# Performance work log

Measured on AMD Instinct MI355X. Metric: run time of the kernel, lower is better.

Reference implementation:

```python
import jax, jax.numpy as jnp
import numpy as np

FP8_MAX = 448.0  # max normal of float8_e4m3fn
NUM_HEADS = 16


def act_quant(x):
    # per-tensor fp8 quantization: scale so max|x| maps to FP8_MAX
    scale = jnp.max(jnp.abs(x)) / FP8_MAX
    q = (x / scale).astype(jnp.float8_e4m3fn)
    return q, scale


def setup_inputs() -> dict:
    key = jax.random.key(0)
    k1, k2, k3, k4 = jax.random.split(key, 4)
    B, S, H = 2, 2048, 2048
    x = jax.random.normal(k1, (B, S, H), dtype=jnp.float32)
    W_qkv = jax.random.normal(k2, (H, 3 * H), dtype=jnp.float32) * (1.0 / np.sqrt(H))
    W_out = jax.random.normal(k3, (H, H), dtype=jnp.float32) * (1.0 / np.sqrt(H))
    b_out = jnp.zeros((H,), dtype=jnp.float32)
    return {"x": x, "W_qkv": W_qkv, "W_out": W_out, "b_out": b_out}


def reference(x, W_qkv, W_out, b_out):
    B, S, H = x.shape
    nH = NUM_HEADS
    hd = H // nH  # 128, matches head_dim default used for scaling

    qkv = jnp.einsum('bsh,hf->bsf', x, W_qkv)          # [B,S,3H]
    qkv = qkv.reshape(B, S, 3, nH, hd)
    q = qkv[:, :, 0].transpose(0, 2, 1, 3)             # [B,nH,S,hd]
    k = qkv[:, :, 1].transpose(0, 2, 1, 3)
    v = qkv[:, :, 2].transpose(0, 2, 1, 3)

    q8, q_scale = act_quant(q)
    k8, k_scale = act_quant(k)
    # fp8_gemm_optimized: dequantized GEMM = (a @ b) * a_scale * b_scale
    scores = jnp.einsum('bhqd,bhkd->bhqk',
                        q8.astype(jnp.float32), k8.astype(jnp.float32))
    scores = scores * (q_scale * k_scale) / jnp.sqrt(jnp.float32(hd))

    attn = jax.nn.softmax(scores, axis=-1)             # [B,nH,S,S]
    # (dropout omitted: deterministic / eval mode)

    v8, v_scale = act_quant(v)
    out = jnp.einsum('bhqk,bhkd->bhqd', attn, v8.astype(jnp.float32))
    out = out * v_scale                                # a_scale = 1 for attn weights

    out = out.transpose(0, 2, 1, 3).reshape(B, S, H)
    return jnp.einsum('bsh,ho->bso', out, W_out) + b_out
```

## Files before the change

kernel.cpp:

```cpp
#include <hip/hip_runtime.h>
#include <hip/hip_bf16.h>
#include <math.h>

#define B_   2
#define S_   2048
#define H_   2048
#define NH   16
#define HD   128
#define ROWS (B_ * S_)
#define F3   (3 * H_)
#define KS   2048

typedef _Float16 f16x8 __attribute__((ext_vector_type(8)));
typedef float    f32x4  __attribute__((ext_vector_type(4)));
typedef float    f32x16 __attribute__((ext_vector_type(16)));

union H2 { unsigned u; _Float16 h[2]; };
union H4 { ushort4 s4; _Float16 h[4]; };
union H4b { uint2 u2; _Float16 h[4]; };
union PU { unsigned u[4]; f16x8 v8; };

__device__ __forceinline__ void gl_lds16(const void* g, void* l) {
  __builtin_amdgcn_global_load_lds(
      (const __attribute__((address_space(1))) void*)g,
      (__attribute__((address_space(3))) void*)l, 16, 0, 0);
}

__device__ __forceinline__ float quant_e4m3(float x) {
  float ax = fabsf(x);
  float q;
  if (ax < 0.015625f) {
    q = rintf(ax * 512.0f) * (1.0f / 512.0f);
  } else {
    unsigned eb = __float_as_uint(ax) & 0x7f800000u;
    float quantum = __uint_as_float(eb - (3u << 23));
    q = rintf(ax / quantum) * quantum;
    if (q > 448.0f) q = 448.0f;
  }
  return copysignf(q, x);
}

__global__ __launch_bounds__(256) void prep_split(
    const float* __restrict__ x, const float* __restrict__ Wqkv,
    _Float16* __restrict__ A1hi, _Float16* __restrict__ A1lo,
    _Float16* __restrict__ B1thi, _Float16* __restrict__ B1tlo) {
  __shared__ _Float16 ht[64][72];
  __shared__ _Float16 lt[64][72];
  const int t = threadIdx.x;
  const int bid = blockIdx.x;
  if (bid < 8192) {
    const size_t i = (size_t)bid * 256 + t;
    float4 v = ((const float4*)x)[i];
    H4 h, l;
    h.h[0] = (_Float16)v.x; l.h[0] = (_Float16)(v.x - (float)h.h[0]);
    h.h[1] = (_Float16)v.y; l.h[1] = (_Float16)(v.y - (float)h.h[1]);
    h.h[2] = (_Float16)v.z; l.h[2] = (_Float16)(v.z - (float)h.h[2]);
    h.h[3] = (_Float16)v.w; l.h[3] = (_Float16)(v.w - (float)h.h[3]);
    ((ushort4*)A1hi)[i] = h.s4;
    ((ushort4*)A1lo)[i] = l.s4;
  } else {
    const int idx = bid - 8192;
    const int n0 = (idx % 96) * 64, k0 = (idx / 96) * 64;
    const int K = H_, N = F3;
#pragma unroll
    for (int p = 0; p < 4; p++) {
      const int k = p * 16 + (t >> 4);
      const int n = (t & 15) * 4;
      float4 v = *(const float4*)(Wqkv + (size_t)(k0 + k) * N + n0 + n);
      _Float16 h0 = (_Float16)v.x, h1 = (_Float16)v.y,
               h2 = (_Float16)v.z, h3 = (_Float16)v.w;
      ht[n + 0][k] = h0; lt[n + 0][k] = (_Float16)(v.x - (float)h0);
      ht[n + 1][k] = h1; lt[n + 1][k] = (_Float16)(v.y - (float)h1);
      ht[n + 2][k] = h2; lt[n + 2][k] = (_Float16)(v.z - (float)h2);
      ht[n + 3][k] = h3; lt[n + 3][k] = (_Float16)(v.w - (float)h3);
    }
    __syncthreads();
#pragma unroll
    for (int it = 0; it < 2; it++) {
      const int idx2 = it * 256 + t;
      const int r = idx2 >> 3, c = (idx2 & 7) * 8;
      *(uint4*)(B1thi + (size_t)(n0 + r) * K + k0 + c) = *(const uint4*)&ht[r][c];
      *(uint4*)(B1tlo + (size_t)(n0 + r) * K + k0 + c) = *(const uint4*)&lt[r][c];
    }
  }
}

__global__ __launch_bounds__(256) void split_tr(
    const float* __restrict__ in, _Float16* __restrict__ hi,
    _Float16* __restrict__ lo, int K, int N) {
  __shared__ _Float16 ht[64][72];
  __shared__ _Float16 lt[64][72];
  const int t = threadIdx.x;
  const int n0 = blockIdx.x * 64, k0 = blockIdx.y * 64;
#pragma unroll
  for (int p = 0; p < 4; p++) {
    const int k = p * 16 + (t >> 4);
    const int n = (t & 15) * 4;
    float4 v = *(const float4*)(in + (size_t)(k0 + k) * N + n0 + n);
    _Float16 h0 = (_Float16)v.x, h1 = (_Float16)v.y,
             h2 = (_Float16)v.z, h3 = (_Float16)v.w;
    ht[n + 0][k] = h0; lt[n + 0][k] = (_Float16)(v.x - (float)h0);
    ht[n + 1][k] = h1; lt[n + 1][k] = (_Float16)(v.y - (float)h1);
    ht[n + 2][k] = h2; lt[n + 2][k] = (_Float16)(v.z - (float)h2);
    ht[n + 3][k] = h3; lt[n + 3][k] = (_Float16)(v.w - (float)h3);
  }
  __syncthreads();
#pragma unroll
  for (int it = 0; it < 2; it++) {
    const int idx = it * 256 + t;
    const int r = idx >> 3, c = (idx & 7) * 8;
    *(uint4*)(hi + (size_t)(n0 + r) * K + k0 + c) = *(const uint4*)&ht[r][c];
    *(uint4*)(lo + (size_t)(n0 + r) * K + k0 + c) = *(const uint4*)&lt[r][c];
  }
}

#define STAGE_A(tt, dst) do {                                                  \
    const _Float16* As_ = ((tt) < 64) ? Ahi : Alo;                             \
    const size_t so_ = (size_t)(row0 + wave * 8 + srow) * KS +                 \
                       (((tt) & 31) << 6) + schunk;                            \
    _Float16* db_ = (dst) + wave * 512;                                        \
    gl_lds16(As_ + so_,                    db_);                               \
    gl_lds16(As_ + so_ + (size_t)64 * KS,  db_ + 4096);                        \
    gl_lds16(As_ + so_ + (size_t)128 * KS, db_ + 8192);                       \
    gl_lds16(As_ + so_ + (size_t)192 * KS, db_ + 12288);                       \
  } while (0)

#define STAGE_B(tt, dst) do {                                                  \
    const _Float16* Bs_ = ((((tt) >> 5)) == 1) ? Btlo : Bthi;                  \
    const size_t so_ = (size_t)(col0 + wave * 8 + srow) * KS +                 \
                       (((tt) & 31) << 6) + schunk;                            \
    _Float16* db_ = (dst) + 16384 + wave * 512;                                \
    gl_lds16(Bs_ + so_,                    db_);                               \
    gl_lds16(Bs_ + so_ + (size_t)64 * KS,  db_ + 4096);                        \
  } while (0)

__global__ __launch_bounds__(512, 2) void gemm_split256(
    const _Float16* __restrict__ Ahi, const _Float16* __restrict__ Alo,
    const _Float16* __restrict__ Bthi, const _Float16* __restrict__ Btlo,
    float* __restrict__ C, const float* __restrict__ bias,
    unsigned* mx, int N, int has_bias) {
  __shared__ __align__(16) _Float16 lds[73728];
  const int t = threadIdx.x;
  const int wave = t >> 6, lane = t & 63;
  const int l15 = lane & 15, g = lane >> 4;
  const int wm = wave >> 1, wn = wave & 1;

  const int gx = gridDim.x;
  const int nwg = gx * gridDim.y;
  const int bid = blockIdx.y * gx + blockIdx.x;
  const int tile = (bid & 7) * (nwg >> 3) + (bid >> 3);
  const int row0 = (tile / gx) * 256, col0 = (tile % gx) * 128;

  const int srow = lane >> 3;
  const int schunk = ((lane & 7) ^ srow) << 3;

  f32x4 acc[4][4] = {};

  _Float16* bufA = lds;
  _Float16* bufB = lds + 24576;
  _Float16* bufC = lds + 49152;

  STAGE_A(0, bufA);
  STAGE_B(0, bufA);
  STAGE_A(1, bufB);
  STAGE_B(1, bufB);
  asm volatile("s_waitcnt vmcnt(6)" ::: "memory");
  __builtin_amdgcn_s_barrier();

  for (int kc = 0; kc < 96; kc++) {
    const _Float16* Ab = bufA;
    const _Float16* Bb = bufA + 16384;
    f16x8 af0[4], bf0[4];
#pragma unroll
    for (int i = 0; i < 4; i++) {
      const int r_ = wm * 64 + i * 16 + l15;
      af0[i] = *(const f16x8*)(Ab + r_ * 64 + ((g ^ (r_ & 7)) << 3));
    }
#pragma unroll
    for (int j = 0; j < 4; j++) {
      const int r_ = wn * 64 + j * 16 + l15;
      bf0[j] = *(const f16x8*)(Bb + r_ * 64 + ((g ^ (r_ & 7)) << 3));
    }
    if (kc + 2 < 96) STAGE_A(kc + 2, bufC);
    __builtin_amdgcn_s_barrier();
    asm volatile("s_waitcnt lgkmcnt(0)" ::: "memory");
    __builtin_amdgcn_sched_barrier(0);
    __builtin_amdgcn_s_setprio(1);
#pragma unroll
    for (int i = 0; i < 4; i++)
#pragma unroll
      for (int j = 0; j < 4; j++)
        acc[i][j] = __builtin_amdgcn_mfma_f32_16x16x32_f16(af0[i], bf0[j], acc[i][j], 0, 0, 0);
    __builtin_amdgcn_s_setprio(0);
    __builtin_amdgcn_s_barrier();
    f16x8 af1[4], bf1[4];
#pragma unroll
    for (int i = 0; i < 4; i++) {
      const int r_ = wm * 64 + i * 16 + l15;
      af1[i] = *(const f16x8*)(Ab + r_ * 64 + (((4 ^ g) ^ (r_ & 7)) << 3));
    }
#pragma unroll
    for (int j = 0; j < 4; j++) {
      const int r_ = wn * 64 + j * 16 + l15;
      bf1[j] = *(const f16x8*)(Bb + r_ * 64 + (((4 ^ g) ^ (r_ & 7)) << 3));
    }
    if (kc + 2 < 96) STAGE_B(kc + 2, bufC);
    __builtin_amdgcn_s_barrier();
    asm volatile("s_waitcnt lgkmcnt(0)" ::: "memory");
    __builtin_amdgcn_sched_barrier(0);
    __builtin_amdgcn_s_setprio(1);
#pragma unroll
    for (int i = 0; i < 4; i++)
#pragma unroll
      for (int j = 0; j < 4; j++)
        acc[i][j] = __builtin_amdgcn_mfma_f32_16x16x32_f16(af1[i], bf1[j], acc[i][j], 0, 0, 0);
    __builtin_amdgcn_s_setprio(0);
    if (kc < 94) { asm volatile("s_waitcnt vmcnt(6)" ::: "memory"); }
    else         { asm volatile("s_waitcnt vmcnt(0)" ::: "memory"); }
    __builtin_amdgcn_s_barrier();
    _Float16* tmp = bufA; bufA = bufB; bufB = bufC; bufC = tmp;
  }

  float bmax = 0.0f;
#pragma unroll
  for (int j = 0; j < 4; j++) {
    const int col = col0 + wn * 64 + j * 16 + l15;
    const float bv = has_bias ? bias[col] : 0.0f;
#pragma unroll
    for (int i = 0; i < 4; i++) {
      const int rbase = row0 + wm * 64 + i * 16 + g * 4;
#pragma unroll
      for (int r = 0; r < 4; r++) {
        const float v = acc[i][j][r] + bv;
        C[(size_t)(rbase + r) * N + col] = v;
        bmax = fmaxf(bmax, fabsf(v));
      }
    }
  }

  if (mx) {
    __syncthreads();
    float* red = (float*)lds;
    red[t] = bmax;
    __syncthreads();
    for (int s2 = 256; s2 > 0; s2 >>= 1) {
      if (t < s2) red[t] = fmaxf(red[t], red[t + s2]);
      __syncthreads();
    }
    if (t == 0) atomicMax(mx + (col0 >> 11), __float_as_uint(red[0]));
  }
}

__global__ __launch_bounds__(256) void quant_qkv(
    const float* __restrict__ qkv, const unsigned* __restrict__ mx,
    _Float16* __restrict__ q8, _Float16* __restrict__ k8,
    _Float16* __restrict__ v8t) {
  __shared__ _Float16 tile[64 * 72];
  const int t = threadIdx.x;
  const int bid = blockIdx.x;

  if (bid < 16384) {
    const size_t base = ((size_t)bid * 256 + t) * 4;
    const int row = (int)(base >> 12);
    const int col = (int)(base & 4095);
    const int seg = col >> 11;
    const int c2 = col & 2047;
    const int h = c2 >> 7, d = c2 & 127;
    const int b = row >> 11, s = row & 2047;
    const float scale = __uint_as_float(mx[seg]) / 448.0f;
    float4 v = *(const float4*)(qkv + (size_t)row * F3 + col);
    H4 r;
    r.h[0] = (_Float16)quant_e4m3(v.x / scale);
    r.h[1] = (_Float16)quant_e4m3(v.y / scale);
    r.h[2] = (_Float16)quant_e4m3(v.z / scale);
    r.h[3] = (_Float16)quant_e4m3(v.w / scale);
    _Float16* dst = seg ? k8 : q8;
    const size_t di = ((size_t)((b * NH + h) * S_) + s) * HD + d;
    *(ushort4*)(dst + di) = r.s4;
  } else {
    const int bt = bid - 16384;
    const int dtile = bt & 1;
    const int stile = (bt >> 1) & 31;
    const int bh = bt >> 6;
    const int b = bh >> 4, h = bh & 15;
    const int s0 = stile * 64, d0 = dtile * 64;
    const float scale = __uint_as_float(mx[2]) / 448.0f;

#pragma unroll
    for (int r = 0; r < 4; r++) {
      const int s = s0 + r * 16 + (t >> 4);
      const int dl = (t & 15) * 4;
      float4 v = *(const float4*)(qkv + (size_t)(b * S_ + s) * F3 + 4096 + h * HD + d0 + dl);
      tile[(dl + 0) * 72 + r * 16 + (t >> 4)] = (_Float16)quant_e4m3(v.x / scale);
      tile[(dl + 1) * 72 + r * 16 + (t >> 4)] = (_Float16)quant_e4m3(v.y / scale);
      tile[(dl + 2) * 72 + r * 16 + (t >> 4)] = (_Float16)quant_e4m3(v.z / scale);
      tile[(dl + 3) * 72 + r * 16 + (t >> 4)] = (_Float16)quant_e4m3(v.w / scale);
    }
    __syncthreads();
#pragma unroll
    for (int j = 0; j < 2; j++) {
      const int wi = j * 256 + t;
      const int dl = wi >> 3;
      const int sch = (wi & 7) * 8;
      uint4 val = *(const uint4*)(tile + dl * 72 + sch);
      *(uint4*)(v8t + (size_t)bh * (HD * S_) + (size_t)(d0 + dl) * S_ + s0 + sch) = val;
    }
  }
}

__global__ __launch_bounds__(256, 2) void attn_kernel(
    const _Float16* __restrict__ q8, const _Float16* __restrict__ k8,
    const _Float16* __restrict__ v8t, const unsigned* __restrict__ mx,
    _Float16* __restrict__ oHi, _Float16* __restrict__ oLo) {
  __shared__ __align__(16) char ldsb[65536];

  const int t = threadIdx.x;
  const int wave = t >> 6;
  const int lane = t & 63;
  const int l31 = lane & 31;
  const int hf = lane >> 5;

  const int qt = blockIdx.x & 15;
  const int bh = blockIdx.x >> 4;
  const int b = bh >> 4, h = bh & 15;
  const int q0 = qt * 128 + wave * 32;

  const float qs = __uint_as_float(mx[0]) * (1.0f / 448.0f);
  const float ks = __uint_as_float(mx[1]) * (1.0f / 448.0f);
  const float vs = __uint_as_float(mx[2]) * (1.0f / 448.0f);
  const float sfac = qs * ks * 0.08838834764831843f;

  f16x8 qf[8];
  {
    const _Float16* qp = q8 + ((size_t)(bh * S_) + q0 + l31) * HD + hf * 8;
#pragma unroll
    for (int st = 0; st < 8; st++)
      qf[st] = *(const f16x8*)(qp + st * 16);
  }

  f32x16 acc[4] = {};
  float m_base = 0.0f;
  float l_run = 0.0f;

  const size_t kB_ = (size_t)(bh * S_) * HD;
  const size_t vB_ = (size_t)bh * (HD * S_);
  const int k_key = t >> 4;
  const int k_dch = (t & 15) * 8;
  const int k_wch = (((t & 15) ^ (k_key & 7)) << 3);
  const int v_d   = t >> 3;
  const int v_sch = (t & 7) * 8;
  const int v_wch = (((t & 7) ^ (v_d & 7)) << 3);

  const int NT = S_ / 64;
  uint4 kp[4], vp[4];

#pragma unroll
  for (int r = 0; r < 4; r++)
    kp[r] = *(const uint4*)(k8 + kB_ + (size_t)(r * 16 + k_key) * HD + k_dch);
#pragma unroll
  for (int r = 0; r < 4; r++)
    vp[r] = *(const uint4*)(v8t + vB_ + (size_t)(r * 32 + v_d) * S_ + v_sch);
  {
    _Float16* K0 = (_Float16*)ldsb;
    _Float16* V0 = (_Float16*)(ldsb + 32768);
#pragma unroll
    for (int r = 0; r < 4; r++)
      *(uint4*)(K0 + (r * 16 + k_key) * 128 + k_wch) = kp[r];
#pragma unroll
    for (int r = 0; r < 4; r++)
      *(uint4*)(V0 + (r * 32 + v_d) * 64 + v_wch) = vp[r];
  }
#pragma unroll
  for (int r = 0; r < 4; r++)
    kp[r] = *(const uint4*)(k8 + kB_ + (size_t)(64 + r * 16 + k_key) * HD + k_dch);
#pragma unroll
  for (int r = 0; r < 4; r++)
    vp[r] = *(const uint4*)(v8t + vB_ + (size_t)(r * 32 + v_d) * S_ + 64 + v_sch);
  __syncthreads();

  for (int kt = 0; kt < NT; kt++) {
    const _Float16* Klds  = (const _Float16*)(ldsb + (kt & 1) * 16384);
    const _Float16* VTlds = (const _Float16*)(ldsb + 32768 + (kt & 1) * 16384);
    if (kt + 1 < NT) {
      _Float16* Kn = (_Float16*)(ldsb + ((kt + 1) & 1) * 16384);
      _Float16* Vn = (_Float16*)(ldsb + 32768 + ((kt + 1) & 1) * 16384);
#pragma unroll
      for (int r = 0; r < 4; r++)
        *(uint4*)(Kn + (r * 16 + k_key) * 128 + k_wch) = kp[r];
#pragma unroll
      for (int r = 0; r < 4; r++)
        *(uint4*)(Vn + (r * 32 + v_d) * 64 + v_wch) = vp[r];
    }
    if (kt + 2 < NT) {
      const int nk = (kt + 2) * 64;
#pragma unroll
      for (int r = 0; r < 4; r++)
        kp[r] = *(const uint4*)(k8 + kB_ + (size_t)(nk + r * 16 + k_key) * HD + k_dch);
#pragma unroll
      for (int r = 0; r < 4; r++)
        vp[r] = *(const uint4*)(v8t + vB_ + (size_t)(r * 32 + v_d) * S_ + nk + v_sch);
    }

#pragma unroll
    for (int sub = 0; sub < 2; sub++) {
      const int ksub = sub * 32;
      f32x16 s = {};
      __builtin_amdgcn_s_setprio(1);
#pragma unroll
      for (int st = 0; st < 8; st++) {
        const int krow = ksub + l31;
        f16x8 af = *(const f16x8*)(Klds + krow * 128 +
                                   (((st * 2 + hf) ^ (krow & 7)) << 3));
        s = __builtin_amdgcn_mfma_f32_32x32x16_f16(af, qf[st], s, 0, 0, 0);
      }
      __builtin_amdgcn_s_setprio(0);
      f16x8 vf0 = *(const f16x8*)(VTlds + l31 * 64 +
                                  (((sub * 4 + 0 * 2 + hf) ^ (l31 & 7)) << 3));
      f16x8 vf1 = *(const f16x8*)(VTlds + l31 * 64 +
                                  (((sub * 4 + 1 * 2 + hf) ^ (l31 & 7)) << 3));
      float p[16];
      if (kt == 0 && sub == 0) {
        float tmax = -3.0e38f;
#pragma unroll
        for (int i = 0; i < 16; i++) {
          p[i] = s[i] * sfac;
          tmax = fmaxf(tmax, p[i]);
        }
        tmax = fmaxf(tmax, __shfl_xor(tmax, 32));
        m_base = tmax;
        float rs = 0.0f;
#pragma unroll
        for (int i = 0; i < 16; i++) {
          p[i] = __expf(p[i] - tmax);
          rs += p[i];
        }
        l_run += rs;
      } else {
        const float mb = m_base;
        float rs = 0.0f;
#pragma unroll
        for (int i = 0; i < 16; i++) {
          p[i] = fminf(__expf(fmaf(s[i], sfac, -mb)), 60000.0f);
          rs += p[i];
        }
        l_run += rs;
      }
      f16x8 pf[2];
#pragma unroll
      for (int c = 0; c < 2; c++) {
        const int c8 = c * 8;
        const int sidx = hf ? 0 : 4;
        const int oidx = hf ? 4 : 0;
        H2 s0h, s1h, o0h, o1h;
        s0h.h[0] = (_Float16)p[c8 + sidx];     s0h.h[1] = (_Float16)p[c8 + sidx + 1];
        s1h.h[0] = (_Float16)p[c8 + sidx + 2]; s1h.h[1] = (_Float16)p[c8 + sidx + 3];
        o0h.h[0] = (_Float16)p[c8 + oidx];     o0h.h[1] = (_Float16)p[c8 + oidx + 1];
        o1h.h[0] = (_Float16)p[c8 + oidx + 2]; o1h.h[1] = (_Float16)p[c8 + oidx + 3];
        unsigned r0 = (unsigned)__shfl_xor((int)s0h.u, 32);
        unsigned r1 = (unsigned)__shfl_xor((int)s1h.u, 32);
        PU pu;
        if (hf == 0) { pu.u[0] = o0h.u; pu.u[1] = o1h.u; pu.u[2] = r0; pu.u[3] = r1; }
        else         { pu.u[0] = r0;    pu.u[1] = r1;    pu.u[2] = o0h.u; pu.u[3] = o1h.u; }
        pf[c] = pu.v8;
      }
#pragma unroll
      for (int dt = 0; dt < 4; dt++) {
        f16x8 nf0, nf1;
        if (dt < 3) {
          const int vrow = (dt + 1) * 32 + l31;
          nf0 = *(const f16x8*)(VTlds + vrow * 64 +
                                (((sub * 4 + 0 * 2 + hf) ^ (vrow & 7)) << 3));
          nf1 = *(const f16x8*)(VTlds + vrow * 64 +
                                (((sub * 4 + 1 * 2 + hf) ^ (vrow & 7)) << 3));
        }
        __builtin_amdgcn_s_setprio(1);
        acc[dt] = __builtin_amdgcn_mfma_f32_32x32x16_f16(vf0, pf[0], acc[dt], 0, 0, 0);
        acc[dt] = __builtin_amdgcn_mfma_f32_32x32x16_f16(vf1, pf[1], acc[dt], 0, 0, 0);
        __builtin_amdgcn_s_setprio(0);
        vf0 = nf0; vf1 = nf1;
      }
    }
    __syncthreads();
  }

  l_run += __shfl_xor(l_run, 32);
  const float f = vs / l_run;

  _Float16* obuf = (_Float16*)ldsb;
  const int obase = wave * 4352;
#pragma unroll
  for (int pass = 0; pass < 2; pass++) {
    __syncthreads();
#pragma unroll
    for (int dt = 0; dt < 4; dt++) {
#pragma unroll
      for (int iq = 0; iq < 4; iq++) {
        const int dl0 = 8 * iq + 4 * hf;
        H4b w;
#pragma unroll
        for (int e = 0; e < 4; e++) {
          const float o = acc[dt][iq * 4 + e] * f;
          const _Float16 hh = (_Float16)o;
          w.h[e] = pass ? (_Float16)(o - (float)hh) : hh;
        }
        *(uint2*)&obuf[obase + l31 * 136 + dt * 32 + dl0] = w.u2;
      }
    }
    __syncthreads();
    _Float16* dst = pass ? oLo : oHi;
#pragma unroll
    for (int ii = 0; ii < 8; ii++) {
      const int qrow = ii * 4 + (lane >> 4);
      const int ch = (lane & 15) * 8;
      uint4 val = *(const uint4*)&obuf[obase + qrow * 136 + ch];
      const size_t ofs = (size_t)(b * S_ + q0 + qrow) * H_ + h * HD + ch;
      *(uint4*)(dst + ofs) = val;
    }
  }
}

extern "C" void kernel_launch(void* const* d_in, const int* in_sizes, int n_in,
                              void* d_out, int out_size, void* d_ws, size_t ws_size,
                              hipStream_t stream) {
  const float* x     = (const float*)d_in[0];
  const float* W_qkv = (const float*)d_in[1];
  const float* W_out = (const float*)d_in[2];
  const float* b_out = (const float*)d_in[3];
  float* out = (float*)d_out;

  char* ws = (char*)d_ws;
  float*    qkv    = (float*)ws;
  _Float16* A2hi   = (_Float16*)(ws + 33554432);
  _Float16* A2lo   = (_Float16*)(ws + 50331648);
  _Float16* B2thi  = (_Float16*)(ws + 67108864);
  _Float16* B2tlo  = (_Float16*)(ws + 75497472);
  _Float16* B1thi  = (_Float16*)(ws + 100663296);
  _Float16* B1tlo  = (_Float16*)(ws + 125829120);
  _Float16* q8     = (_Float16*)(ws + 100663296);
  _Float16* k8     = (_Float16*)(ws + 117440512);
  _Float16* v8t    = (_Float16*)(ws + 134217728);
  _Float16* A1hi   = (_Float16*)(ws + 150994944);
  _Float16* A1lo   = (_Float16*)(ws + 167772160);
  unsigned* mx     = (unsigned*)(ws + 184549376);

  hipMemsetAsync(mx, 0, 3 * sizeof(unsigned), stream);

  prep_split<<<11264, 256, 0, stream>>>(x, W_qkv, A1hi, A1lo, B1thi, B1tlo);

  gemm_split256<<<dim3(F3 / 128, ROWS / 256), 512, 0, stream>>>(
      A1hi, A1lo, B1thi, B1tlo, qkv, nullptr, mx, F3, 0);

  quant_qkv<<<16384 + B_ * NH * 32 * 2, 256, 0, stream>>>(qkv, mx, q8, k8, v8t);

  attn_kernel<<<B_ * NH * 16, 256, 0, stream>>>(q8, k8, v8t, mx, A2hi, A2lo);

  split_tr<<<dim3(H_ / 64, H_ / 64), 256, 0, stream>>>(W_out, B2thi, B2tlo, H_, H_);

  gemm_split256<<<dim3(H_ / 128, ROWS / 256), 512, 0, stream>>>(
      A2hi, A2lo, B2thi, B2tlo, out, b_out, nullptr, H_, 1);
}
```

Measured before the change: 784.4 us.

## Merge GEMM half-steps and batch both attention key sub-tiles per iteration

In the GEMM main loop, all A/B fragments for both k-halves are now loaded up front and both stage copies issued together. This removes two of the three barriers, the lgkmcnt waits, sched_barriers and setprio toggles per iteration. In the attention kernel, the two 32-key sub-tiles are computed together: both QK^T accumulators are interleaved, softmax runs for both, then the PV MFMAs are issued in one loop. This raises instruction-level parallelism but also register pressure, which could lower occupancy or cause spills.

```diff
diff --git a/kernel.cpp b/kernel.cpp
--- a/kernel.cpp
+++ b/kernel.cpp
@@ -170,51 +170,33 @@
   for (int kc = 0; kc < 96; kc++) {
     const _Float16* Ab = bufA;
     const _Float16* Bb = bufA + 16384;
-    f16x8 af0[4], bf0[4];
+    f16x8 af0[4], bf0[4], af1[4], bf1[4];
 #pragma unroll
     for (int i = 0; i < 4; i++) {
       const int r_ = wm * 64 + i * 16 + l15;
       af0[i] = *(const f16x8*)(Ab + r_ * 64 + ((g ^ (r_ & 7)) << 3));
+      af1[i] = *(const f16x8*)(Ab + r_ * 64 + (((4 ^ g) ^ (r_ & 7)) << 3));
     }
 #pragma unroll
     for (int j = 0; j < 4; j++) {
       const int r_ = wn * 64 + j * 16 + l15;
       bf0[j] = *(const f16x8*)(Bb + r_ * 64 + ((g ^ (r_ & 7)) << 3));
-    }
-    if (kc + 2 < 96) STAGE_A(kc + 2, bufC);
-    __builtin_amdgcn_s_barrier();
-    asm volatile("s_waitcnt lgkmcnt(0)" ::: "memory");
-    __builtin_amdgcn_sched_barrier(0);
-    __builtin_amdgcn_s_setprio(1);
+      bf1[j] = *(const f16x8*)(Bb + r_ * 64 + (((4 ^ g) ^ (r_ & 7)) << 3));
+    }
+    if (kc + 2 < 96) {
+      STAGE_A(kc + 2, bufC);
+      STAGE_B(kc + 2, bufC);
+    }
 #pragma unroll
     for (int i = 0; i < 4; i++)
 #pragma unroll
       for (int j = 0; j < 4; j++)
         acc[i][j] = __builtin_amdgcn_mfma_f32_16x16x32_f16(af0[i], bf0[j], acc[i][j], 0, 0, 0);
-    __builtin_amdgcn_s_setprio(0);
-    __builtin_amdgcn_s_barrier();
-    f16x8 af1[4], bf1[4];
-#pragma unroll
-    for (int i = 0; i < 4; i++) {
-      const int r_ = wm * 64 + i * 16 + l15;
-      af1[i] = *(const f16x8*)(Ab + r_ * 64 + (((4 ^ g) ^ (r_ & 7)) << 3));
-    }
-#pragma unroll
-    for (int j = 0; j < 4; j++) {
-      const int r_ = wn * 64 + j * 16 + l15;
-      bf1[j] = *(const f16x8*)(Bb + r_ * 64 + (((4 ^ g) ^ (r_ & 7)) << 3));
-    }
-    if (kc + 2 < 96) STAGE_B(kc + 2, bufC);
-    __builtin_amdgcn_s_barrier();
-    asm volatile("s_waitcnt lgkmcnt(0)" ::: "memory");
-    __builtin_amdgcn_sched_barrier(0);
-    __builtin_amdgcn_s_setprio(1);
 #pragma unroll
     for (int i = 0; i < 4; i++)
 #pragma unroll
       for (int j = 0; j < 4; j++)
         acc[i][j] = __builtin_amdgcn_mfma_f32_16x16x32_f16(af1[i], bf1[j], acc[i][j], 0, 0, 0);
-    __builtin_amdgcn_s_setprio(0);
     if (kc < 94) { asm volatile("s_waitcnt vmcnt(6)" ::: "memory"); }
     else         { asm volatile("s_waitcnt vmcnt(0)" ::: "memory"); }
     __builtin_amdgcn_s_barrier();
@@ -401,61 +383,79 @@
         vp[r] = *(const uint4*)(v8t + vB_ + (size_t)(r * 32 + v_d) * S_ + nk + v_sch);
     }
 
-#pragma unroll
-    for (int sub = 0; sub < 2; sub++) {
-      const int ksub = sub * 32;
-      f32x16 s = {};
-      __builtin_amdgcn_s_setprio(1);
-#pragma unroll
-      for (int st = 0; st < 8; st++) {
-        const int krow = ksub + l31;
-        f16x8 af = *(const f16x8*)(Klds + krow * 128 +
-                                   (((st * 2 + hf) ^ (krow & 7)) << 3));
-        s = __builtin_amdgcn_mfma_f32_32x32x16_f16(af, qf[st], s, 0, 0, 0);
-      }
-      __builtin_amdgcn_s_setprio(0);
-      f16x8 vf0 = *(const f16x8*)(VTlds + l31 * 64 +
-                                  (((sub * 4 + 0 * 2 + hf) ^ (l31 & 7)) << 3));
-      f16x8 vf1 = *(const f16x8*)(VTlds + l31 * 64 +
-                                  (((sub * 4 + 1 * 2 + hf) ^ (l31 & 7)) << 3));
-      float p[16];
-      if (kt == 0 && sub == 0) {
-        float tmax = -3.0e38f;
-#pragma unroll
-        for (int i = 0; i < 16; i++) {
-          p[i] = s[i] * sfac;
-          tmax = fmaxf(tmax, p[i]);
-        }
-        tmax = fmaxf(tmax, __shfl_xor(tmax, 32));
-        m_base = tmax;
-        float rs = 0.0f;
-#pragma unroll
-        for (int i = 0; i < 16; i++) {
-          p[i] = __expf(p[i] - tmax);
-          rs += p[i];
-        }
-        l_run += rs;
-      } else {
-        const float mb = m_base;
-        float rs = 0.0f;
-#pragma unroll
-        for (int i = 0; i < 16; i++) {
-          p[i] = fminf(__expf(fmaf(s[i], sfac, -mb)), 60000.0f);
-          rs += p[i];
-        }
-        l_run += rs;
-      }
-      f16x8 pf[2];
+    f32x16 s0 = {}, s1 = {};
+    __builtin_amdgcn_s_setprio(1);
+#pragma unroll
+    for (int st = 0; st < 8; st++) {
+      const int kr0 = l31;
+      const int kr1 = 32 + l31;
+      f16x8 a0 = *(const f16x8*)(Klds + kr0 * 128 +
+                                 (((st * 2 + hf) ^ (kr0 & 7)) << 3));
+      f16x8 a1 = *(const f16x8*)(Klds + kr1 * 128 +
+                                 (((st * 2 + hf) ^ (kr1 & 7)) << 3));
+      s0 = __builtin_amdgcn_mfma_f32_32x32x16_f16(a0, qf[st], s0, 0, 0, 0);
+      s1 = __builtin_amdgcn_mfma_f32_32x32x16_f16(a1, qf[st], s1, 0, 0, 0);
+    }
+    __builtin_amdgcn_s_setprio(0);
+
+    f16x8 vf00 = *(const f16x8*)(VTlds + l31 * 64 + (((0 + hf) ^ (l31 & 7)) << 3));
+    f16x8 vf01 = *(const f16x8*)(VTlds + l31 * 64 + (((2 + hf) ^ (l31 & 7)) << 3));
+    f16x8 vf10 = *(const f16x8*)(VTlds + l31 * 64 + (((4 + hf) ^ (l31 & 7)) << 3));
+    f16x8 vf11 = *(const f16x8*)(VTlds + l31 * 64 + (((6 + hf) ^ (l31 & 7)) << 3));
+
+    float p0[16], p1[16];
+    if (kt == 0) {
+      float tmax = -3.0e38f;
+#pragma unroll
+      for (int i = 0; i < 16; i++) {
+        p0[i] = s0[i] * sfac;
+        tmax = fmaxf(tmax, p0[i]);
+      }
+      tmax = fmaxf(tmax, __shfl_xor(tmax, 32));
+      m_base = tmax;
+      float rs = 0.0f;
+#pragma unroll
+      for (int i = 0; i < 16; i++) {
+        p0[i] = __expf(p0[i] - tmax);
+        rs += p0[i];
+      }
+      l_run += rs;
+    } else {
+      const float mb = m_base;
+      float rs = 0.0f;
+#pragma unroll
+      for (int i = 0; i < 16; i++) {
+        p0[i] = fminf(__expf(fmaf(s0[i], sfac, -mb)), 60000.0f);
+        rs += p0[i];
+      }
+      l_run += rs;
+    }
+    {
+      const float mb = m_base;
+      float rs = 0.0f;
+#pragma unroll
+      for (int i = 0; i < 16; i++) {
+        p1[i] = fminf(__expf(fmaf(s1[i], sfac, -mb)), 60000.0f);
+        rs += p1[i];
+      }
+      l_run += rs;
+    }
+
+    f16x8 pf0[2], pf1[2];
+#pragma unroll
+    for (int sb = 0; sb < 2; sb++) {
+      const float* pp = sb ? p1 : p0;
+      f16x8* pf = sb ? pf1 : pf0;
 #pragma unroll
       for (int c = 0; c < 2; c++) {
         const int c8 = c * 8;
         const int sidx = hf ? 0 : 4;
         const int oidx = hf ? 4 : 0;
         H2 s0h, s1h, o0h, o1h;
-        s0h.h[0] = (_Float16)p[c8 + sidx];     s0h.h[1] = (_Float16)p[c8 + sidx + 1];
-        s1h.h[0] = (_Float16)p[c8 + sidx + 2]; s1h.h[1] = (_Float16)p[c8 + sidx + 3];
-        o0h.h[0] = (_Float16)p[c8 + oidx];     o0h.h[1] = (_Float16)p[c8 + oidx + 1];
-        o1h.h[0] = (_Float16)p[c8 + oidx + 2]; o1h.h[1] = (_Float16)p[c8 + oidx + 3];
+        s0h.h[0] = (_Float16)pp[c8 + sidx];     s0h.h[1] = (_Float16)pp[c8 + sidx + 1];
+        s1h.h[0] = (_Float16)pp[c8 + sidx + 2]; s1h.h[1] = (_Float16)pp[c8 + sidx + 3];
+        o0h.h[0] = (_Float16)pp[c8 + oidx];     o0h.h[1] = (_Float16)pp[c8 + oidx + 1];
+        o1h.h[0] = (_Float16)pp[c8 + oidx + 2]; o1h.h[1] = (_Float16)pp[c8 + oidx + 3];
         unsigned r0 = (unsigned)__shfl_xor((int)s0h.u, 32);
         unsigned r1 = (unsigned)__shfl_xor((int)s1h.u, 32);
         PU pu;
@@ -463,22 +463,25 @@
         else         { pu.u[0] = r0;    pu.u[1] = r1;    pu.u[2] = o0h.u; pu.u[3] = o1h.u; }
         pf[c] = pu.v8;
       }
-#pragma unroll
-      for (int dt = 0; dt < 4; dt++) {
-        f16x8 nf0, nf1;
-        if (dt < 3) {
-          const int vrow = (dt + 1) * 32 + l31;
-          nf0 = *(const f16x8*)(VTlds + vrow * 64 +
-                                (((sub * 4 + 0 * 2 + hf) ^ (vrow & 7)) << 3));
-          nf1 = *(const f16x8*)(VTlds + vrow * 64 +
-                                (((sub * 4 + 1 * 2 + hf) ^ (vrow & 7)) << 3));
-        }
-        __builtin_amdgcn_s_setprio(1);
-        acc[dt] = __builtin_amdgcn_mfma_f32_32x32x16_f16(vf0, pf[0], acc[dt], 0, 0, 0);
-        acc[dt] = __builtin_amdgcn_mfma_f32_32x32x16_f16(vf1, pf[1], acc[dt], 0, 0, 0);
-        __builtin_amdgcn_s_setprio(0);
-        vf0 = nf0; vf1 = nf1;
-      }
+    }
+
+#pragma unroll
+    for (int dt = 0; dt < 4; dt++) {
+      f16x8 n00, n01, n10, n11;
+      if (dt < 3) {
+        const int vrow = (dt + 1) * 32 + l31;
+        n00 = *(const f16x8*)(VTlds + vrow * 64 + (((0 + hf) ^ (vrow & 7)) << 3));
+        n01 = *(const f16x8*)(VTlds + vrow * 64 + (((2 + hf) ^ (vrow & 7)) << 3));
+        n10 = *(const f16x8*)(VTlds + vrow * 64 + (((4 + hf) ^ (vrow & 7)) << 3));
+        n11 = *(const f16x8*)(VTlds + vrow * 64 + (((6 + hf) ^ (vrow & 7)) << 3));
+      }
+      __builtin_amdgcn_s_setprio(1);
+      acc[dt] = __builtin_amdgcn_mfma_f32_32x32x16_f16(vf00, pf0[0], acc[dt], 0, 0, 0);
+      acc[dt] = __builtin_amdgcn_mfma_f32_32x32x16_f16(vf01, pf0[1], acc[dt], 0, 0, 0);
+      acc[dt] = __builtin_amdgcn_mfma_f32_32x32x16_f16(vf10, pf1[0], acc[dt], 0, 0, 0);
+      acc[dt] = __builtin_amdgcn_mfma_f32_32x32x16_f16(vf11, pf1[1], acc[dt], 0, 0, 0);
+      __builtin_amdgcn_s_setprio(0);
+      vf00 = n00; vf01 = n01; vf10 = n10; vf11 = n11;
     }
     __syncthreads();
   }
```

Result: faster. 718.3 us (-8.4%).
